# Optimization experiments

Hardware: AMD Instinct MI355X
Metric: run time of the kernel (lower is better)

The kernel has to match this reference:

```python
import jax, jax.numpy as jnp
from jax import lax
import numpy as np

B, T, H, C = 64, 512, 1024, 21


def setup_inputs() -> dict:
    key = jax.random.key(0)
    k1, k2, k3, k4 = jax.random.split(key, 4)
    return {
        "sequence_output": jax.random.normal(k1, (B, T, H), dtype=jnp.float32),
        "input_mask": jax.random.randint(k2, (B, T), 0, 2, dtype=jnp.int32),
        "W": jax.random.normal(k3, (H, C), dtype=jnp.float32) * 0.02,
        "b": jnp.zeros((C,), dtype=jnp.float32),
        "transitions": jax.random.normal(k4, (C, C), dtype=jnp.float32) * 0.1,
    }


def crf_decode(logits, transitions, seq_len):
    """Viterbi decode matching tfa.text.crf_decode semantics (length-masked)."""
    Bb, Tt, Cc = logits.shape
    ident = jnp.arange(Cc, dtype=jnp.int32)[None, :]  # identity backpointers

    def fwd_step(state, inp):
        logit_t, t = inp  # [B,C], scalar step index
        scores = state[:, :, None] + transitions[None, :, :]  # [B, C_prev, C_cur]
        bp = jnp.argmax(scores, axis=1).astype(jnp.int32)      # [B, C]
        new_state = jnp.max(scores, axis=1) + logit_t          # [B, C]
        valid = (t < seq_len)[:, None]                          # [B, 1]
        state = jnp.where(valid, new_state, state)
        bp = jnp.where(valid, bp, ident)
        return state, bp

    ts = jnp.arange(1, Tt)
    xs = (jnp.transpose(logits[:, 1:], (1, 0, 2)), ts)
    final_state, bps = lax.scan(fwd_step, logits[:, 0], xs)  # bps: [T-1, B, C]
    last_tag = jnp.argmax(final_state, axis=-1).astype(jnp.int32)  # [B]

    def back_step(tag, bp_t):
        tag = jnp.take_along_axis(bp_t, tag[:, None], axis=1)[:, 0]
        return tag, tag

    _, tags_rev = lax.scan(back_step, last_tag, bps, reverse=True)  # [T-1, B]
    tags = jnp.concatenate([tags_rev, last_tag[None, :]], axis=0)   # [T, B]
    return jnp.transpose(tags, (1, 0))  # [B, T]


def reference(sequence_output, input_mask, W, b, transitions):
    # classifier logits
    logits = jnp.einsum("bth,hc->btc", sequence_output, W) + b  # [B,T,C]
    mask = (input_mask == 1).astype(jnp.int32)
    seq_len = jnp.sum(mask, axis=-1)  # [B]
    decode_tags = crf_decode(logits, transitions, seq_len)
    return jax.nn.one_hot(decode_tags, logits.shape[-1], dtype=jnp.float32), logits
```

## Files before the change

### kernel.cpp

```cpp
#include <hip/hip_runtime.h>
#include <stdint.h>

#define BB 64
#define TT 512
#define HH 1024
#define CC 21

#define GAS __attribute__((address_space(1)))
#define LAS __attribute__((address_space(3)))
__device__ __forceinline__ void gll16(const void* g, void* l) {
    __builtin_amdgcn_global_load_lds((const GAS uint32_t*)g, (LAS uint32_t*)l, 16, 0, 0);
}

#define RL(x, lane) __uint_as_float(__builtin_amdgcn_readlane(__float_as_uint(x), (lane)))

__global__ __launch_bounds__(512) void logits_kernel(
    const float* __restrict__ seq,
    const float* __restrict__ W,
    const float* __restrict__ bias,
    float* __restrict__ logits)
{
    __shared__ float comb[7][64][25];

    const int t = threadIdx.x;
    const int w = __builtin_amdgcn_readfirstlane(t >> 6);
    const int l = t & 63;
    const int row0 = blockIdx.x * 64;
    const float* xrow  = seq + (size_t)(row0 + l) * HH + w * 128;
    const float* wbase = W + (size_t)w * 128 * CC;

    float acc[CC];
#pragma unroll
    for (int c = 0; c < CC; ++c) acc[c] = 0.f;

    float4 xb0 = *(const float4*)(xrow);
    float4 xb1 = *(const float4*)(xrow + 4);

#pragma unroll 2
    for (int s = 0; s < 32; ++s) {
        float4 xv = (s & 1) ? xb1 : xb0;
        if (s + 2 < 32) {
            float4 nv = *(const float4*)(xrow + (s + 2) * 4);
            if (s & 1) xb1 = nv; else xb0 = nv;
        }
        const float* wp = wbase + s * 84;
#pragma unroll
        for (int j = 0; j < 4; ++j) {
            float xc = (&xv.x)[j];
#pragma unroll
            for (int c = 0; c < CC; ++c)
                acc[c] += xc * wp[j * CC + c];
        }
    }

    if (w > 0) {
        float* cr = &comb[w - 1][l][0];
#pragma unroll
        for (int c = 0; c < CC; ++c) cr[c] = acc[c];
    }
    __syncthreads();
    if (w == 0) {
        float* orow = logits + (size_t)(row0 + l) * CC;
#pragma unroll
        for (int c = 0; c < CC; ++c) {
            float s = acc[c] + bias[c];
#pragma unroll
            for (int i = 0; i < 7; ++i) s += comb[i][l][c];
            orow[c] = s;
        }
    }
}

__global__ __launch_bounds__(256) void viterbi_kernel(
    const float* __restrict__ logits,
    const int* __restrict__ mask,
    const float* __restrict__ trans,
    float* __restrict__ onehot)
{
    __shared__ __align__(16) float lg[(TT + 2) * CC];
    __shared__ float stS[TT * CC];
    __shared__ float trL[CC * CC];
    __shared__ unsigned char bp[TT * CC];
    __shared__ unsigned char tagl[TT];
    __shared__ unsigned char mapl[12 * CC];
    __shared__ unsigned char bnd[13];

    const int tid = threadIdx.x;
    const int w = tid >> 6;
    const int l = tid & 63;
    const int b = blockIdx.x;

    const float* lb = logits + (size_t)b * TT * CC;
    for (int i = w; i < 42; i += 4)
        gll16(lb + (size_t)(i * 64 + l) * 4, &lg[i * 256]);

    for (int j = tid; j < CC * CC; j += 256) trL[j] = trans[j];

    int sl = 0;
#pragma unroll
    for (int k = 0; k < 8; ++k) sl += mask[b * TT + k * 64 + l];
#pragma unroll
    for (int o = 32; o > 0; o >>= 1) sl += __shfl_xor(sl, o);
    const int idstart = (sl >= 1) ? (sl - 1) : 0;

    asm volatile("s_waitcnt vmcnt(0)" ::: "memory");
    __syncthreads();

    if (w == 0) {
        const bool act = (l < CC);
        if (act) {
            const int cc = l;
            float tcol[CC];
#pragma unroll
            for (int cp = 0; cp < CC; ++cp) tcol[cp] = trL[cp * CC + cc];

            float st = lg[cc];
            stS[l] = st;
            int lgo = CC + cc;
            float lg1 = lg[lgo];
            float lg2 = lg[lgo + CC];
            int sto = CC + l;

#pragma unroll 1
            for (int t = 1; t < sl; ++t) {
                float sc[CC];
#pragma unroll
                for (int cp = 0; cp < CC; ++cp) sc[cp] = RL(st, cp) + tcol[cp];
                float m0 = fmaxf(fmaxf(sc[0], sc[1]), sc[2]);
                float m1 = fmaxf(fmaxf(sc[3], sc[4]), sc[5]);
                float m2 = fmaxf(fmaxf(sc[6], sc[7]), sc[8]);
                float m3 = fmaxf(fmaxf(sc[9], sc[10]), sc[11]);
                float m4 = fmaxf(fmaxf(sc[12], sc[13]), sc[14]);
                float m5 = fmaxf(fmaxf(sc[15], sc[16]), sc[17]);
                float m6 = fmaxf(fmaxf(sc[18], sc[19]), sc[20]);
                float n0 = fmaxf(fmaxf(m0, m1), m2);
                float n1 = fmaxf(fmaxf(m3, m4), m5);
                float best = fmaxf(fmaxf(n0, n1), m6);
                st = best + lg1;
                lg1 = lg2;
                lg2 = lg[lgo + 2 * CC];
                lgo += CC;
                stS[sto] = st;
                sto += CC;
            }

            float fs[CC];
#pragma unroll
            for (int cp = 0; cp < CC; ++cp) fs[cp] = RL(st, cp);
            float q0 = fmaxf(fmaxf(fs[0], fs[1]), fs[2]);
            float q1 = fmaxf(fmaxf(fs[3], fs[4]), fs[5]);
            float q2 = fmaxf(fmaxf(fs[6], fs[7]), fs[8]);
            float q3 = fmaxf(fmaxf(fs[9], fs[10]), fs[11]);
            float q4 = fmaxf(fmaxf(fs[12], fs[13]), fs[14]);
            float q5 = fmaxf(fmaxf(fs[15], fs[16]), fs[17]);
            float q6 = fmaxf(fmaxf(fs[18], fs[19]), fs[20]);
            float fbest = fmaxf(fmaxf(fmaxf(q0, q1), fmaxf(q2, q3)),
                                fmaxf(fmaxf(q4, q5), q6));
            int e[CC];
#pragma unroll
            for (int cp = 0; cp < CC; ++cp) e[cp] = (fs[cp] == fbest) ? cp : 63;
            int i0 = min(min(e[0], e[1]), e[2]);
            int i1 = min(min(e[3], e[4]), e[5]);
            int i2 = min(min(e[6], e[7]), e[8]);
            int i3 = min(min(e[9], e[10]), e[11]);
            int i4 = min(min(e[12], e[13]), e[14]);
            int i5 = min(min(e[15], e[16]), e[17]);
            int i6 = min(min(e[18], e[19]), e[20]);
            int last = min(min(min(i0, i1), min(i2, i3)), min(min(i4, i5), i6));
            if (l == 0) tagl[TT - 1] = (unsigned char)last;
        }
    } else {
        int s = (w - 1) * 64 + l;
        if (s < 189) {
            int c0 = s % CC, prow = s / CC;
#pragma unroll 1
            for (int p = idstart + prow; p < TT; p += 9)
                bp[p * CC + c0] = (unsigned char)c0;
        }
    }
    __syncthreads();

    if (tid < 252) {
        const int c0 = tid % CC, tg = tid / CC;
        float tc[CC];
#pragma unroll
        for (int cp = 0; cp < CC; ++cp) tc[cp] = trL[cp * CC + c0];
#pragma unroll 1
        for (int t = 1 + tg; t < sl; t += 12) {
            const float* sp = stS + (t - 1) * CC;
            float bv = sp[0] + tc[0];
            int bi = 0;
#pragma unroll
            for (int cp = 1; cp < CC; ++cp) {
                float v = sp[cp] + tc[cp];
                bool g = v > bv;
                bv = g ? v : bv;
                bi = g ? cp : bi;
            }
            bp[(t - 1) * CC + c0] = (unsigned char)bi;
        }
    }
    __syncthreads();

    if (tid < 252) {
        int g = tid / CC, cand = tid % CC;
        int endp = g * 43;
        int startp = min(g * 43 + 42, TT - 2);
        int m = cand;
#pragma unroll 1
        for (int i = 0; i < 43; ++i) {
            int p = startp - i;
            int pr = (p >= endp) ? p : endp;
            int m2 = bp[pr * CC + m];
            m = (p >= endp) ? m2 : m;
        }
        mapl[g * CC + cand] = (unsigned char)m;
    }
    __syncthreads();

    if (tid == 0) {
        int eb = tagl[TT - 1];
        bnd[12] = (unsigned char)eb;
        for (int g = 11; g >= 0; --g) {
            eb = mapl[g * CC + eb];
            bnd[g] = (unsigned char)eb;
        }
    }
    __syncthreads();

    if (tid < 12) {
        int g = tid;
        int endp = g * 43;
        int startp = min(g * 43 + 42, TT - 2);
        int eb = bnd[g + 1];
#pragma unroll 1
        for (int p = startp; p >= endp; --p) {
            eb = bp[p * CC + eb];
            tagl[p] = (unsigned char)eb;
        }
    }
    __syncthreads();

    if (tid < 252) {
        const int c0 = tid % CC, prow = tid / CC;
        float* ob = onehot + (size_t)b * TT * CC;
#pragma unroll 1
        for (int p = prow; p < TT; p += 12)
            ob[(size_t)p * CC + c0] = (c0 == (int)tagl[p]) ? 1.f : 0.f;
    }
}

extern "C" void kernel_launch(void* const* d_in, const int* in_sizes, int n_in,
                              void* d_out, int out_size, void* d_ws, size_t ws_size,
                              hipStream_t stream) {
    const float* seq   = (const float*)d_in[0];
    const int*   msk   = (const int*)d_in[1];
    const float* W     = (const float*)d_in[2];
    const float* bias  = (const float*)d_in[3];
    const float* trans = (const float*)d_in[4];

    float* onehot_out = (float*)d_out;
    float* logits_out = onehot_out + (size_t)BB * TT * CC;

    logits_kernel<<<512, 512, 0, stream>>>(seq, W, bias, logits_out);
    viterbi_kernel<<<BB, 256, 0, stream>>>(logits_out, msk, trans, onehot_out);
}
```

Measured before the change: 146.2 us.

## Process two rows per thread in logits GEMV and broadcast W via readlane

The logits kernel now computes 128 rows per block with two rows per thread, so each W value is reused twice. W is loaded coalesced into registers across the wave and broadcast with readlane instead of each thread reading W from memory. The grid is halved to 256 blocks. The Viterbi forward loop is restructured to run on all 64 lanes with a simpler lookahead logit load, and the lg buffer shrinks by one row. The risk is higher register pressure from the doubled accumulators and fewer blocks to cover the GPU.

```diff
diff --git a/kernel.cpp b/kernel.cpp
--- a/kernel.cpp
+++ b/kernel.cpp
@@ -20,53 +20,100 @@
     const float* __restrict__ bias,
     float* __restrict__ logits)
 {
-    __shared__ float comb[7][64][25];
+    __shared__ float comb[7][128][22];
 
     const int t = threadIdx.x;
-    const int w = __builtin_amdgcn_readfirstlane(t >> 6);
+    const int w = t >> 6;
     const int l = t & 63;
-    const int row0 = blockIdx.x * 64;
-    const float* xrow  = seq + (size_t)(row0 + l) * HH + w * 128;
-    const float* wbase = W + (size_t)w * 128 * CC;
-
-    float acc[CC];
-#pragma unroll
-    for (int c = 0; c < CC; ++c) acc[c] = 0.f;
-
-    float4 xb0 = *(const float4*)(xrow);
-    float4 xb1 = *(const float4*)(xrow + 4);
+    const int row0 = blockIdx.x * 128;
+    const int h0 = w * 128;
+
+    const float* x0 = seq + (size_t)(row0 + l) * HH + h0;
+    const float* x1 = seq + (size_t)(row0 + l + 64) * HH + h0;
+    const float* wb = W + (size_t)h0 * CC;
+
+    float acc0[CC], acc1[CC];
+#pragma unroll
+    for (int c = 0; c < CC; ++c) { acc0[c] = 0.f; acc1[c] = 0.f; }
+
+    float4 xa[4], xbv[4], xan[4], xbn[4];
+    float wr[6], wrn[6];
+
+#pragma unroll
+    for (int k = 0; k < 4; ++k) {
+        xa[k]  = *(const float4*)(x0 + k * 4);
+        xbv[k] = *(const float4*)(x1 + k * 4);
+    }
+#pragma unroll
+    for (int i = 0; i < 6; ++i) {
+        int j = i * 64 + l;
+        wr[i] = (j < 16 * CC) ? wb[j] : 0.f;
+    }
 
 #pragma unroll 2
-    for (int s = 0; s < 32; ++s) {
-        float4 xv = (s & 1) ? xb1 : xb0;
-        if (s + 2 < 32) {
-            float4 nv = *(const float4*)(xrow + (s + 2) * 4);
-            if (s & 1) xb1 = nv; else xb0 = nv;
-        }
-        const float* wp = wbase + s * 84;
-#pragma unroll
-        for (int j = 0; j < 4; ++j) {
-            float xc = (&xv.x)[j];
-#pragma unroll
-            for (int c = 0; c < CC; ++c)
-                acc[c] += xc * wp[j * CC + c];
+    for (int ch = 0; ch < 8; ++ch) {
+        if (ch < 7) {
+            const float* px0 = x0 + (ch + 1) * 16;
+            const float* px1 = x1 + (ch + 1) * 16;
+#pragma unroll
+            for (int k = 0; k < 4; ++k) {
+                xan[k] = *(const float4*)(px0 + k * 4);
+                xbn[k] = *(const float4*)(px1 + k * 4);
+            }
+            const float* pw = wb + (ch + 1) * 16 * CC;
+#pragma unroll
+            for (int i = 0; i < 6; ++i) {
+                int j = i * 64 + l;
+                wrn[i] = (j < 16 * CC) ? pw[j] : 0.f;
+            }
+        }
+
+#pragma unroll
+        for (int g = 0; g < 4; ++g) {
+#pragma unroll
+            for (int j = 0; j < 4; ++j) {
+                float xv0 = (&xa[g].x)[j];
+                float xv1 = (&xbv[g].x)[j];
+#pragma unroll
+                for (int c = 0; c < CC; ++c) {
+                    const int idx = (g * 4 + j) * CC + c;
+                    float s = RL(wr[idx >> 6], idx & 63);
+                    acc0[c] = fmaf(s, xv0, acc0[c]);
+                    acc1[c] = fmaf(s, xv1, acc1[c]);
+                }
+            }
+        }
+
+        if (ch < 7) {
+#pragma unroll
+            for (int k = 0; k < 4; ++k) { xa[k] = xan[k]; xbv[k] = xbn[k]; }
+#pragma unroll
+            for (int i = 0; i < 6; ++i) wr[i] = wrn[i];
         }
     }
 
     if (w > 0) {
-        float* cr = &comb[w - 1][l][0];
-#pragma unroll
-        for (int c = 0; c < CC; ++c) cr[c] = acc[c];
+#pragma unroll
+        for (int c = 0; c < CC; ++c) {
+            comb[w - 1][l][c]      = acc0[c];
+            comb[w - 1][l + 64][c] = acc1[c];
+        }
     }
     __syncthreads();
     if (w == 0) {
-        float* orow = logits + (size_t)(row0 + l) * CC;
+        float* o0 = logits + (size_t)(row0 + l) * CC;
+        float* o1 = logits + (size_t)(row0 + l + 64) * CC;
 #pragma unroll
         for (int c = 0; c < CC; ++c) {
-            float s = acc[c] + bias[c];
-#pragma unroll
-            for (int i = 0; i < 7; ++i) s += comb[i][l][c];
-            orow[c] = s;
+            float s0 = acc0[c] + bias[c];
+            float s1 = acc1[c] + bias[c];
+#pragma unroll
+            for (int i = 0; i < 7; ++i) {
+                s0 += comb[i][l][c];
+                s1 += comb[i][l + 64][c];
+            }
+            o0[c] = s0;
+            o1[c] = s1;
         }
     }
 }
@@ -77,7 +124,7 @@
     const float* __restrict__ trans,
     float* __restrict__ onehot)
 {
-    __shared__ __align__(16) float lg[(TT + 2) * CC];
+    __shared__ __align__(16) float lg[(TT + 1) * CC];
     __shared__ float stS[TT * CC];
     __shared__ float trL[CC * CC];
     __shared__ unsigned char bp[TT * CC];
@@ -108,67 +155,60 @@
 
     if (w == 0) {
         const bool act = (l < CC);
-        if (act) {
-            const int cc = l;
-            float tcol[CC];
-#pragma unroll
-            for (int cp = 0; cp < CC; ++cp) tcol[cp] = trL[cp * CC + cc];
-
-            float st = lg[cc];
-            stS[l] = st;
-            int lgo = CC + cc;
-            float lg1 = lg[lgo];
-            float lg2 = lg[lgo + CC];
-            int sto = CC + l;
-
-#pragma unroll 1
-            for (int t = 1; t < sl; ++t) {
-                float sc[CC];
-#pragma unroll
-                for (int cp = 0; cp < CC; ++cp) sc[cp] = RL(st, cp) + tcol[cp];
-                float m0 = fmaxf(fmaxf(sc[0], sc[1]), sc[2]);
-                float m1 = fmaxf(fmaxf(sc[3], sc[4]), sc[5]);
-                float m2 = fmaxf(fmaxf(sc[6], sc[7]), sc[8]);
-                float m3 = fmaxf(fmaxf(sc[9], sc[10]), sc[11]);
-                float m4 = fmaxf(fmaxf(sc[12], sc[13]), sc[14]);
-                float m5 = fmaxf(fmaxf(sc[15], sc[16]), sc[17]);
-                float m6 = fmaxf(fmaxf(sc[18], sc[19]), sc[20]);
-                float n0 = fmaxf(fmaxf(m0, m1), m2);
-                float n1 = fmaxf(fmaxf(m3, m4), m5);
-                float best = fmaxf(fmaxf(n0, n1), m6);
-                st = best + lg1;
-                lg1 = lg2;
-                lg2 = lg[lgo + 2 * CC];
-                lgo += CC;
-                stS[sto] = st;
-                sto += CC;
-            }
-
-            float fs[CC];
-#pragma unroll
-            for (int cp = 0; cp < CC; ++cp) fs[cp] = RL(st, cp);
-            float q0 = fmaxf(fmaxf(fs[0], fs[1]), fs[2]);
-            float q1 = fmaxf(fmaxf(fs[3], fs[4]), fs[5]);
-            float q2 = fmaxf(fmaxf(fs[6], fs[7]), fs[8]);
-            float q3 = fmaxf(fmaxf(fs[9], fs[10]), fs[11]);
-            float q4 = fmaxf(fmaxf(fs[12], fs[13]), fs[14]);
-            float q5 = fmaxf(fmaxf(fs[15], fs[16]), fs[17]);
-            float q6 = fmaxf(fmaxf(fs[18], fs[19]), fs[20]);
-            float fbest = fmaxf(fmaxf(fmaxf(q0, q1), fmaxf(q2, q3)),
-                                fmaxf(fmaxf(q4, q5), q6));
-            int e[CC];
-#pragma unroll
-            for (int cp = 0; cp < CC; ++cp) e[cp] = (fs[cp] == fbest) ? cp : 63;
-            int i0 = min(min(e[0], e[1]), e[2]);
-            int i1 = min(min(e[3], e[4]), e[5]);
-            int i2 = min(min(e[6], e[7]), e[8]);
-            int i3 = min(min(e[9], e[10]), e[11]);
-            int i4 = min(min(e[12], e[13]), e[14]);
-            int i5 = min(min(e[15], e[16]), e[17]);
-            int i6 = min(min(e[18], e[19]), e[20]);
-            int last = min(min(min(i0, i1), min(i2, i3)), min(min(i4, i5), i6));
-            if (l == 0) tagl[TT - 1] = (unsigned char)last;
-        }
+        const int cc = act ? l : 0;
+        float tcol[CC];
+#pragma unroll
+        for (int cp = 0; cp < CC; ++cp) tcol[cp] = trL[cp * CC + cc];
+
+        float st = lg[cc];
+        if (act) stS[l] = st;
+        float lgt_next = lg[CC + cc];
+
+#pragma unroll 1
+        for (int t = 1; t < sl; ++t) {
+            float lgt = lgt_next;
+            lgt_next = lg[(t + 1) * CC + cc];
+            float sc[CC];
+#pragma unroll
+            for (int cp = 0; cp < CC; ++cp) sc[cp] = RL(st, cp) + tcol[cp];
+            float m0 = fmaxf(fmaxf(sc[0], sc[1]), sc[2]);
+            float m1 = fmaxf(fmaxf(sc[3], sc[4]), sc[5]);
+            float m2 = fmaxf(fmaxf(sc[6], sc[7]), sc[8]);
+            float m3 = fmaxf(fmaxf(sc[9], sc[10]), sc[11]);
+            float m4 = fmaxf(fmaxf(sc[12], sc[13]), sc[14]);
+            float m5 = fmaxf(fmaxf(sc[15], sc[16]), sc[17]);
+            float m6 = fmaxf(fmaxf(sc[18], sc[19]), sc[20]);
+            float n0 = fmaxf(fmaxf(m0, m1), m2);
+            float n1 = fmaxf(fmaxf(m3, m4), m5);
+            float best = fmaxf(fmaxf(n0, n1), m6);
+            st = best + lgt;
+            if (act) stS[t * CC + l] = st;
+        }
+
+        float fs[CC];
+#pragma unroll
+        for (int cp = 0; cp < CC; ++cp) fs[cp] = RL(st, cp);
+        float q0 = fmaxf(fmaxf(fs[0], fs[1]), fs[2]);
+        float q1 = fmaxf(fmaxf(fs[3], fs[4]), fs[5]);
+        float q2 = fmaxf(fmaxf(fs[6], fs[7]), fs[8]);
+        float q3 = fmaxf(fmaxf(fs[9], fs[10]), fs[11]);
+        float q4 = fmaxf(fmaxf(fs[12], fs[13]), fs[14]);
+        float q5 = fmaxf(fmaxf(fs[15], fs[16]), fs[17]);
+        float q6 = fmaxf(fmaxf(fs[18], fs[19]), fs[20]);
+        float fbest = fmaxf(fmaxf(fmaxf(q0, q1), fmaxf(q2, q3)),
+                            fmaxf(fmaxf(q4, q5), q6));
+        int e[CC];
+#pragma unroll
+        for (int cp = 0; cp < CC; ++cp) e[cp] = (fs[cp] == fbest) ? cp : 63;
+        int i0 = min(min(e[0], e[1]), e[2]);
+        int i1 = min(min(e[3], e[4]), e[5]);
+        int i2 = min(min(e[6], e[7]), e[8]);
+        int i3 = min(min(e[9], e[10]), e[11]);
+        int i4 = min(min(e[12], e[13]), e[14]);
+        int i5 = min(min(e[15], e[16]), e[17]);
+        int i6 = min(min(e[18], e[19]), e[20]);
+        int last = min(min(min(i0, i1), min(i2, i3)), min(min(i4, i5), i6));
+        if (l == 0) tagl[TT - 1] = (unsigned char)last;
     } else {
         int s = (w - 1) * 64 + l;
         if (s < 189) {
@@ -262,6 +302,6 @@
     float* onehot_out = (float*)d_out;
     float* logits_out = onehot_out + (size_t)BB * TT * CC;
 
-    logits_kernel<<<512, 512, 0, stream>>>(seq, W, bias, logits_out);
+    logits_kernel<<<256, 512, 0, stream>>>(seq, W, bias, logits_out);
     viterbi_kernel<<<BB, 256, 0, stream>>>(logits_out, msk, trans, onehot_out);
 }
```

New measurement: 135.0 us. -7.7%, faster.
